# Kernel tuning notes

Hardware: AMD Instinct MI355X
Metric: run time of the kernel (lower is better)

The kernel has to match this reference:

```python
import jax, jax.numpy as jnp
import numpy as np

G = 256          # voxel grid extent per axis
N = 30000        # number of active voxels
CHANNELS = [(4,16),(16,16),(16,32),(32,32),(32,32),(32,64),(64,64),(64,64),(64,64),(64,64),(64,64),(64,64),(64,128)]
BN_EPS = 1e-3

_OFFS = np.array([[i, j, k] for i in (-1, 0, 1) for j in (-1, 0, 1) for k in (-1, 0, 1)], dtype=np.int32)  # 27 kernel taps


def setup_inputs() -> dict:
    key = jax.random.key(0)
    ks = jax.random.split(key, 2 + len(CHANNELS))
    rng = np.random.default_rng(0)
    # unique active voxel coordinates in [0, G)^3
    c = rng.integers(0, G, size=(2 * N, 3))
    c = np.unique(c, axis=0)
    rng.shuffle(c)
    coords = jnp.asarray(c[:N], dtype=jnp.int32)
    inp = {
        "voxel_features": jax.random.normal(ks[0], (N, CHANNELS[0][0]), jnp.float32),
        "coords": coords,
    }
    for i, (ci, co) in enumerate(CHANNELS):
        inp[f"W{i}"] = jax.random.normal(ks[1 + i], (27, ci, co), jnp.float32) * (1.0 / np.sqrt(27.0 * ci))
        inp[f"g{i}"] = jnp.ones((co,), jnp.float32)
        inp[f"b{i}"] = jnp.zeros((co,), jnp.float32)
    return inp


def _neighbors(coords):
    """Build rulebook: for each of 27 taps, index of neighbor voxel (or masked)."""
    n = coords.shape[0]
    grid = jnp.full((G, G, G), -1, jnp.int32).at[coords[:, 0], coords[:, 1], coords[:, 2]].set(
        jnp.arange(n, dtype=jnp.int32))
    offs = jnp.asarray(_OFFS)
    nc = coords[None, :, :] + offs[:, None, :]               # [27, N, 3]
    inb = jnp.all((nc >= 0) & (nc < G), axis=-1)             # [27, N]
    ncc = jnp.clip(nc, 0, G - 1)
    nidx = grid[ncc[..., 0], ncc[..., 1], ncc[..., 2]]       # [27, N]
    valid = (inb & (nidx >= 0)).astype(jnp.float32)
    return jnp.maximum(nidx, 0), valid


def _sconv(feat, W, nidx, valid):
    # gather-GEMM: gathered [27, N, Cin] -> out [N, Cout]
    g = feat[nidx] * valid[..., None]
    return jnp.einsum('knc,kcd->nd', g, W)


def _bn_relu(x, g, b):
    m = jnp.mean(x, axis=0)
    v = jnp.var(x, axis=0)
    return jax.nn.relu((x - m) * jax.lax.rsqrt(v + BN_EPS) * g + b)


def reference(voxel_features, coords,
              W0, W1, W2, W3, W4, W5, W6, W7, W8, W9, W10, W11, W12,
              g0, g1, g2, g3, g4, g5, g6, g7, g8, g9, g10, g11, g12,
              b0, b1, b2, b3, b4, b5, b6, b7, b8, b9, b10, b11, b12):
    Ws = [W0, W1, W2, W3, W4, W5, W6, W7, W8, W9, W10, W11, W12]
    gs = [g0, g1, g2, g3, g4, g5, g6, g7, g8, g9, g10, g11, g12]
    bs = [b0, b1, b2, b3, b4, b5, b6, b7, b8, b9, b10, b11, b12]
    nidx, valid = _neighbors(coords)
    x = voxel_features
    for W, g, b in zip(Ws, gs, bs):
        x = _bn_relu(_sconv(x, W, nidx, valid), g, b)
    return x  # [N, 128] final backbone features
```

## Files before the change

### kernel.cpp

```cpp
#include <hip/hip_runtime.h>
#include <stdint.h>
#include <stddef.h>

#define GG 256

typedef __attribute__((ext_vector_type(8))) short bf16x8;
typedef __attribute__((ext_vector_type(4))) float f32x4;

__device__ __forceinline__ float bf2f(short s) {
  return __builtin_bit_cast(float, ((unsigned)(unsigned short)s) << 16);
}
__device__ __forceinline__ short f2bf(float f) {
  unsigned u = __builtin_bit_cast(unsigned, f);
  unsigned r = (u + 0x7FFFu + ((u >> 16) & 1u)) >> 16;
  return (short)r;
}


__global__ __launch_bounds__(256) void k_clear_grid(uint32_t* g, int n32) {
  int i = blockIdx.x * 256 + threadIdx.x;
  int stride = gridDim.x * 256;
  for (; i < n32; i += stride) g[i] = 0xFFFFFFFFu;
}

__global__ __launch_bounds__(256) void k_scatter(const int* __restrict__ coords,
                                                 uint16_t* __restrict__ grid, int n) {
  int i = blockIdx.x * 256 + threadIdx.x;
  if (i >= n) return;
  int x = coords[3 * i], y = coords[3 * i + 1], z = coords[3 * i + 2];
  grid[(((x << 8) | y) << 8) | z] = (uint16_t)i;
}

__global__ __launch_bounds__(256) void k_rulebook(const int* __restrict__ coords,
                                                  const uint16_t* __restrict__ grid,
                                                  int* __restrict__ nidx, int n) {
  int i = blockIdx.x * 256 + threadIdx.x;
  if (i >= n) return;
  int x = coords[3 * i], y = coords[3 * i + 1], z = coords[3 * i + 2];
  int k = 0;
  for (int dx = -1; dx <= 1; ++dx)
    for (int dy = -1; dy <= 1; ++dy)
      for (int dz = -1; dz <= 1; ++dz) {
        int nx = x + dx, ny = y + dy, nz = z + dz;
        int v = -1;
        if (((nx | ny | nz) >= 0) && nx < GG && ny < GG && nz < GG) {
          uint16_t s = grid[(((nx << 8) | ny) << 8) | nz];
          if (s != 0xFFFFu) v = (int)s;
        }
        nidx[k * n + i] = v;
        ++k;
      }
}


__global__ __launch_bounds__(256) void k_zero(float* __restrict__ stats, float* __restrict__ zp) {
  int i = blockIdx.x * 256 + threadIdx.x;
  if (i < 13 * 256) stats[i] = 0.0f;
  if (i < 64) zp[i] = 0.0f;
}


struct PackArgs {
  const float* W[13];
  short* P[13];
  int ci[13], co[13], nkb[13];
};

__global__ __launch_bounds__(256) void k_pack(PackArgs pa) {
  int L = blockIdx.y;
  int ci = pa.ci[L], co = pa.co[L], nkb = pa.nkb[L];
  int total = nkb * co * 32;
  const float* W = pa.W[L];
  short* P = pa.P[L];
  for (int e = blockIdx.x * 256 + threadIdx.x; e < total; e += gridDim.x * 256) {
    int kk = e & 31;
    int rest = e >> 5;
    int c = rest % co;
    int kb = rest / co;
    int k = kb * 32 + kk;
    int tap = k / ci, cc = k % ci;
    float v = (tap < 27) ? W[((size_t)tap * ci + cc) * co + c] : 0.0f;
    P[e] = f2bf(v);
  }
}


__global__ __launch_bounds__(256) void k_sconv_l0(const float* __restrict__ feat,
                                                  const float* __restrict__ W,
                                                  const int* __restrict__ nidx,
                                                  float* __restrict__ y,
                                                  float* __restrict__ stats, int n) {
  int i = blockIdx.x * 256 + threadIdx.x;
  bool act = i < n;
  int ii = act ? i : (n - 1);
  float acc[16];
#pragma unroll
  for (int c = 0; c < 16; ++c) acc[c] = 0.0f;
  for (int t = 0; t < 27; ++t) {
    int nid = nidx[t * n + ii];
    float4 f = make_float4(0.f, 0.f, 0.f, 0.f);
    if (act && nid >= 0) f = *(const float4*)(feat + 4 * (size_t)nid);
    const float* Wt = W + t * 64;
#pragma unroll
    for (int c = 0; c < 16; ++c)
      acc[c] = fmaf(f.x, Wt[c],
               fmaf(f.y, Wt[16 + c],
               fmaf(f.z, Wt[32 + c],
               fmaf(f.w, Wt[48 + c], acc[c]))));
  }
  if (act) {
    float* o = y + (size_t)i * 16;
#pragma unroll
    for (int c = 0; c < 16; c += 4) *(float4*)(o + c) = make_float4(acc[c], acc[c+1], acc[c+2], acc[c+3]);
  }
  __shared__ float ss[4][16], sq[4][16];
  int w = threadIdx.x >> 6, l = threadIdx.x & 63;
#pragma unroll
  for (int c = 0; c < 16; ++c) {
    float s = act ? acc[c] : 0.0f;
    float q = s * s;
#pragma unroll
    for (int off = 32; off; off >>= 1) {
      s += __shfl_xor(s, off);
      q += __shfl_xor(q, off);
    }
    if (l == 0) { ss[w][c] = s; sq[w][c] = q; }
  }
  __syncthreads();
  if (threadIdx.x < 16) {
    int c = threadIdx.x;
    atomicAdd(&stats[c], ss[0][c] + ss[1][c] + ss[2][c] + ss[3][c]);
    atomicAdd(&stats[16 + c], sq[0][c] + sq[1][c] + sq[2][c] + sq[3][c]);
  }
}


template <int CI, int CO>
__global__ __launch_bounds__(256) void k_sconv_mfma(
    const short* __restrict__ feat, const short* __restrict__ P,
    const int* __restrict__ nidx, const short* __restrict__ zpage,
    short* __restrict__ y, float* __restrict__ stats, int n) {
  constexpr int LOG2CI = (CI == 16) ? 4 : (CI == 32) ? 5 : 6;
  constexpr int NKB = (27 * CI + 31) / 32;
  constexpr int NT = CO / 16;

  const int w = threadIdx.x >> 6;
  const int l = threadIdx.x & 63;
  const int lo = l & 15, g = l >> 4;
  const int bvox = blockIdx.x * 64;
  const int rowg = bvox + 16 * w + lo;
  const int rowc = (rowg < n) ? rowg : (n - 1);

  f32x4 acc[NT];
#pragma unroll
  for (int t = 0; t < NT; ++t) acc[t] = (f32x4){0.f, 0.f, 0.f, 0.f};

  auto loadA = [&](int kb) -> bf16x8 {
    int kg = kb * 32 + 8 * g;
    int tap = kg >> LOG2CI;
    int ch = kg & (CI - 1);
    const short* ap = zpage;
    if (tap < 27) {
      int nid = nidx[tap * n + rowc];
      if (nid >= 0) ap = feat + (size_t)nid * CI + ch;
    }
    return *(const bf16x8*)ap;
  };
  auto loadB = [&](int kb, int t) -> bf16x8 {
    return *(const bf16x8*)(P + ((size_t)(kb * CO + 16 * t + lo)) * 32 + 8 * g);
  };

  bf16x8 a = loadA(0);
  bf16x8 b[NT];
#pragma unroll
  for (int t = 0; t < NT; ++t) b[t] = loadB(0, t);

  for (int kb = 0; kb < NKB - 1; ++kb) {
    bf16x8 an = loadA(kb + 1);
    bf16x8 bn[NT];
#pragma unroll
    for (int t = 0; t < NT; ++t) bn[t] = loadB(kb + 1, t);
#pragma unroll
    for (int t = 0; t < NT; ++t)
      acc[t] = __builtin_amdgcn_mfma_f32_16x16x32_bf16(a, b[t], acc[t], 0, 0, 0);
    a = an;
#pragma unroll
    for (int t = 0; t < NT; ++t) b[t] = bn[t];
  }
#pragma unroll
  for (int t = 0; t < NT; ++t)
    acc[t] = __builtin_amdgcn_mfma_f32_16x16x32_bf16(a, b[t], acc[t], 0, 0, 0);

  __shared__ float ss[4][CO], sq[4][CO];
#pragma unroll
  for (int t = 0; t < NT; ++t) {
    int col = 16 * t + lo;
    float sv = 0.f, qv = 0.f;
#pragma unroll
    for (int r = 0; r < 4; ++r) {
      int row = bvox + 16 * w + 4 * g + r;
      float v = acc[t][r];
      bool valid = row < n;
      if (valid) y[(size_t)row * CO + col] = f2bf(v);
      v = valid ? v : 0.f;
      sv += v;
      qv += v * v;
    }
    sv += __shfl_xor(sv, 16); sv += __shfl_xor(sv, 32);
    qv += __shfl_xor(qv, 16); qv += __shfl_xor(qv, 32);
    if (g == 0) { ss[w][col] = sv; sq[w][col] = qv; }
  }
  __syncthreads();
  for (int c = threadIdx.x; c < CO; c += 256) {
    atomicAdd(&stats[c], ss[0][c] + ss[1][c] + ss[2][c] + ss[3][c]);
    atomicAdd(&stats[CO + c], sq[0][c] + sq[1][c] + sq[2][c] + sq[3][c]);
  }
}


template <int CO, bool INF32, bool OUTF32>
__global__ __launch_bounds__(256) void k_bn_apply(const void* __restrict__ yv,
                                                  const float* __restrict__ stats,
                                                  const float* __restrict__ gam,
                                                  const float* __restrict__ bet,
                                                  void* __restrict__ outv, int n) {
  int idx = blockIdx.x * 256 + threadIdx.x;
  int tot = n * CO / 8;
  if (idx >= tot) return;
  size_t e0 = (size_t)idx * 8;
  int c0 = (int)(e0 & (CO - 1));
  float invn = 1.0f / (float)n;

  float vin[8];
  if (INF32) {
    const float4* p = (const float4*)((const float*)yv + e0);
    float4 u0 = p[0], u1 = p[1];
    vin[0] = u0.x; vin[1] = u0.y; vin[2] = u0.z; vin[3] = u0.w;
    vin[4] = u1.x; vin[5] = u1.y; vin[6] = u1.z; vin[7] = u1.w;
  } else {
    bf16x8 v = *(const bf16x8*)((const short*)yv + e0);
#pragma unroll
    for (int j = 0; j < 8; ++j) vin[j] = bf2f(v[j]);
  }

  float vout[8];
#pragma unroll
  for (int j = 0; j < 8; ++j) {
    int c = c0 + j;
    float m = stats[c] * invn;
    float var = fmaf(-m, m, stats[CO + c] * invn);
    float rstd = rsqrtf(var + 1e-3f);
    float o = fmaf((vin[j] - m) * rstd, gam[c], bet[c]);
    vout[j] = fmaxf(o, 0.0f);
  }

  if (OUTF32) {
    float4* p = (float4*)((float*)outv + e0);
    p[0] = make_float4(vout[0], vout[1], vout[2], vout[3]);
    p[1] = make_float4(vout[4], vout[5], vout[6], vout[7]);
  } else {
    bf16x8 o;
#pragma unroll
    for (int j = 0; j < 8; ++j) o[j] = f2bf(vout[j]);
    *(bf16x8*)((short*)outv + e0) = o;
  }
}


extern "C" void kernel_launch(void* const* d_in, const int* in_sizes, int n_in,
                              void* d_out, int out_size, void* d_ws, size_t ws_size,
                              hipStream_t stream) {
  const float* vf = (const float*)d_in[0];
  const int* coords = (const int*)d_in[1];
  const int n = in_sizes[1] / 3;

  static const int CIs[13] = {4, 16, 16, 32, 32, 32, 64, 64, 64, 64, 64, 64, 64};
  static const int COs[13] = {16, 16, 32, 32, 32, 64, 64, 64, 64, 64, 64, 64, 128};

  char* ws = (char*)d_ws;
  size_t off = 0;
  auto carve = [&](size_t bytes) { void* p = ws + off; off = (off + bytes + 255) & ~(size_t)255; return p; };
  uint16_t* grid = (uint16_t*)carve((size_t)GG * GG * GG * 2);
  int* nidx = (int*)carve((size_t)27 * n * 4);
  short* featA = (short*)carve((size_t)n * 128 * 2);
  short* featB = (short*)carve((size_t)n * 128 * 2);
  short* y = (short*)carve((size_t)n * 128 * 2);
  short* Ppool = (short*)carve((size_t)2 * 1024 * 1024 * 2);
  float* stats = (float*)carve((size_t)13 * 256 * 4);
  float* zpage = (float*)carve(256);

  PackArgs pa;
  {
    size_t poff = 0;
    for (int L = 0; L < 13; ++L) {
      int ci = CIs[L], co = COs[L];
      int nkb = (27 * ci + 31) / 32;
      pa.W[L] = (const float*)d_in[2 + 3 * L];
      pa.P[L] = Ppool + poff;
      pa.ci[L] = ci; pa.co[L] = co; pa.nkb[L] = nkb;
      poff += (size_t)nkb * co * 32;
    }
  }

  const int n32 = GG * GG * GG / 2;
  k_clear_grid<<<2048, 256, 0, stream>>>((uint32_t*)grid, n32);
  k_scatter<<<(n + 255) / 256, 256, 0, stream>>>(coords, grid, n);
  k_rulebook<<<(n + 255) / 256, 256, 0, stream>>>(coords, grid, nidx, n);
  k_zero<<<13, 256, 0, stream>>>(stats, zpage);
  k_pack<<<dim3(128, 13), 256, 0, stream>>>(pa);

  k_sconv_l0<<<(n + 255) / 256, 256, 0, stream>>>(vf, pa.W[0], nidx, (float*)y, stats, n);
  k_bn_apply<16, true, false><<<((n * 16 / 8) + 255) / 256, 256, 0, stream>>>(
      (const void*)y, stats, (const float*)d_in[3], (const float*)d_in[4], (void*)featA, n);

  short* cur = featA;
  short* nxt = featB;
  const int nb64 = (n + 63) / 64;

#define RUN_MFMA(L, CI, CO, LAST)                                                             \
  do {                                                                                        \
    float* st = stats + 256 * (L);                                                            \
    k_sconv_mfma<CI, CO><<<nb64, 256, 0, stream>>>(cur, (const short*)pa.P[L], nidx,          \
                                                   (const short*)zpage, y, st, n);            \
    const float* gg = (const float*)d_in[3 + 3 * (L)];                                        \
    const float* bb = (const float*)d_in[4 + 3 * (L)];                                        \
    int nb = ((n * (CO) / 8) + 255) / 256;                                                    \
    if (LAST) {                                                                               \
      k_bn_apply<CO, false, true><<<nb, 256, 0, stream>>>((const void*)y, st, gg, bb,         \
                                                          (void*)d_out, n);                   \
    } else {                                                                                  \
      k_bn_apply<CO, false, false><<<nb, 256, 0, stream>>>((const void*)y, st, gg, bb,        \
                                                           (void*)nxt, n);                    \
      short* t_ = cur; cur = nxt; nxt = t_;                                                   \
    }                                                                                         \
  } while (0)

  RUN_MFMA(1, 16, 16, false);
  RUN_MFMA(2, 16, 32, false);
  RUN_MFMA(3, 32, 32, false);
  RUN_MFMA(4, 32, 32, false);
  RUN_MFMA(5, 32, 64, false);
  RUN_MFMA(6, 64, 64, false);
  RUN_MFMA(7, 64, 64, false);
  RUN_MFMA(8, 64, 64, false);
  RUN_MFMA(9, 64, 64, false);
  RUN_MFMA(10, 64, 64, false);
  RUN_MFMA(11, 64, 64, false);
  RUN_MFMA(12, 64, 128, true);
#undef RUN_MFMA
}
```

Before: 648.1 us.

## Re-partition sparse conv MFMA kernel across waves and shrink rulebook indices

New measurement: 1.017 ms. +56.9%, slower.

```diff
diff --git a/kernel.cpp b/kernel.cpp
--- a/kernel.cpp
+++ b/kernel.cpp
@@ -3,6 +3,7 @@
 #include <stddef.h>
 
 #define GG 256
+#define STP 16
 
 typedef __attribute__((ext_vector_type(8))) short bf16x8;
 typedef __attribute__((ext_vector_type(4))) float f32x4;
@@ -33,7 +34,7 @@
 
 __global__ __launch_bounds__(256) void k_rulebook(const int* __restrict__ coords,
                                                   const uint16_t* __restrict__ grid,
-                                                  int* __restrict__ nidx, int n) {
+                                                  short* __restrict__ nidx, int n) {
   int i = blockIdx.x * 256 + threadIdx.x;
   if (i >= n) return;
   int x = coords[3 * i], y = coords[3 * i + 1], z = coords[3 * i + 2];
@@ -42,10 +43,10 @@
     for (int dy = -1; dy <= 1; ++dy)
       for (int dz = -1; dz <= 1; ++dz) {
         int nx = x + dx, ny = y + dy, nz = z + dz;
-        int v = -1;
+        short v = -1;
         if (((nx | ny | nz) >= 0) && nx < GG && ny < GG && nz < GG) {
           uint16_t s = grid[(((nx << 8) | ny) << 8) | nz];
-          if (s != 0xFFFFu) v = (int)s;
+          if (s != 0xFFFFu) v = (short)s;
         }
         nidx[k * n + i] = v;
         ++k;
@@ -54,9 +55,9 @@
 
 
 __global__ __launch_bounds__(256) void k_zero(float* __restrict__ stats, float* __restrict__ zp) {
-  int i = blockIdx.x * 256 + threadIdx.x;
-  if (i < 13 * 256) stats[i] = 0.0f;
-  if (i < 64) zp[i] = 0.0f;
+  int tot = 13 * 256 * STP;
+  for (int i = blockIdx.x * 256 + threadIdx.x; i < tot; i += gridDim.x * 256) stats[i] = 0.0f;
+  if (blockIdx.x == 0 && threadIdx.x < 64) zp[threadIdx.x] = 0.0f;
 }
 
 
@@ -87,7 +88,7 @@
 
 __global__ __launch_bounds__(256) void k_sconv_l0(const float* __restrict__ feat,
                                                   const float* __restrict__ W,
-                                                  const int* __restrict__ nidx,
+                                                  const short* __restrict__ nidx,
                                                   float* __restrict__ y,
                                                   float* __restrict__ stats, int n) {
   int i = blockIdx.x * 256 + threadIdx.x;
@@ -129,8 +130,8 @@
   __syncthreads();
   if (threadIdx.x < 16) {
     int c = threadIdx.x;
-    atomicAdd(&stats[c], ss[0][c] + ss[1][c] + ss[2][c] + ss[3][c]);
-    atomicAdd(&stats[16 + c], sq[0][c] + sq[1][c] + sq[2][c] + sq[3][c]);
+    atomicAdd(&stats[c * STP], ss[0][c] + ss[1][c] + ss[2][c] + ss[3][c]);
+    atomicAdd(&stats[(16 + c) * STP], sq[0][c] + sq[1][c] + sq[2][c] + sq[3][c]);
   }
 }
 
@@ -138,22 +139,31 @@
 template <int CI, int CO>
 __global__ __launch_bounds__(256) void k_sconv_mfma(
     const short* __restrict__ feat, const short* __restrict__ P,
-    const int* __restrict__ nidx, const short* __restrict__ zpage,
-    short* __restrict__ y, float* __restrict__ stats, int n) {
+    const short* __restrict__ nidx, const short* __restrict__ zpage,
+    float* __restrict__ y, float* __restrict__ stats, int n) {
   constexpr int LOG2CI = (CI == 16) ? 4 : (CI == 32) ? 5 : 6;
   constexpr int NKB = (27 * CI + 31) / 32;
-  constexpr int NT = CO / 16;
+  constexpr int MT = (CO == 16) ? 4 : (CO == 32) ? 2 : 1;
+  constexpr int WPM = 4 / MT;
+  constexpr int NT = (CO == 128) ? 2 : 1;
+  constexpr int R = MT * 16;
 
   const int w = threadIdx.x >> 6;
   const int l = threadIdx.x & 63;
   const int lo = l & 15, g = l >> 4;
-  const int bvox = blockIdx.x * 64;
-  const int rowg = bvox + 16 * w + lo;
-  const int rowc = (rowg < n) ? rowg : (n - 1);
-
-  f32x4 acc[NT];
-#pragma unroll
-  for (int t = 0; t < NT; ++t) acc[t] = (f32x4){0.f, 0.f, 0.f, 0.f};
+  const int mt = w / WPM;
+  const int nw = w % WPM;
+  const int bvox = blockIdx.x * R;
+
+  __shared__ short nid_s[27][R];
+  for (int idx = threadIdx.x; idx < 27 * R; idx += 256) {
+    int tap = idx / R, r = idx % R;
+    int v = bvox + r;
+    nid_s[tap][r] = (v < n) ? nidx[tap * n + v] : (short)-1;
+  }
+  __syncthreads();
+
+  const int rowl = mt * 16 + lo;
 
   auto loadA = [&](int kb) -> bf16x8 {
     int kg = kb * 32 + 8 * g;
@@ -161,65 +171,76 @@
     int ch = kg & (CI - 1);
     const short* ap = zpage;
     if (tap < 27) {
-      int nid = nidx[tap * n + rowc];
+      int nid = nid_s[tap][rowl];
       if (nid >= 0) ap = feat + (size_t)nid * CI + ch;
     }
     return *(const bf16x8*)ap;
   };
-  auto loadB = [&](int kb, int t) -> bf16x8 {
+  auto loadB = [&](int kb, int j) -> bf16x8 {
+    int t = nw + j * WPM;
     return *(const bf16x8*)(P + ((size_t)(kb * CO + 16 * t + lo)) * 32 + 8 * g);
   };
 
-  bf16x8 a = loadA(0);
-  bf16x8 b[NT];
-#pragma unroll
-  for (int t = 0; t < NT; ++t) b[t] = loadB(0, t);
-
-  for (int kb = 0; kb < NKB - 1; ++kb) {
-    bf16x8 an = loadA(kb + 1);
-    bf16x8 bn[NT];
-#pragma unroll
-    for (int t = 0; t < NT; ++t) bn[t] = loadB(kb + 1, t);
-#pragma unroll
-    for (int t = 0; t < NT; ++t)
-      acc[t] = __builtin_amdgcn_mfma_f32_16x16x32_bf16(a, b[t], acc[t], 0, 0, 0);
-    a = an;
-#pragma unroll
-    for (int t = 0; t < NT; ++t) b[t] = bn[t];
-  }
-#pragma unroll
-  for (int t = 0; t < NT; ++t)
-    acc[t] = __builtin_amdgcn_mfma_f32_16x16x32_bf16(a, b[t], acc[t], 0, 0, 0);
-
-  __shared__ float ss[4][CO], sq[4][CO];
-#pragma unroll
-  for (int t = 0; t < NT; ++t) {
-    int col = 16 * t + lo;
+  f32x4 acc[NT];
+#pragma unroll
+  for (int j = 0; j < NT; ++j) acc[j] = (f32x4){0.f, 0.f, 0.f, 0.f};
+
+  bf16x8 aC = loadA(0), aN = loadA(1);
+  bf16x8 bC[NT], bN[NT];
+#pragma unroll
+  for (int j = 0; j < NT; ++j) { bC[j] = loadB(0, j); bN[j] = loadB(1, j); }
+
+#pragma unroll 2
+  for (int kb = 0; kb < NKB; ++kb) {
+    bf16x8 aP = aC;
+    bf16x8 bP[NT];
+#pragma unroll
+    for (int j = 0; j < NT; ++j) bP[j] = bC[j];
+    if (kb + 2 < NKB) {
+      aP = loadA(kb + 2);
+#pragma unroll
+      for (int j = 0; j < NT; ++j) bP[j] = loadB(kb + 2, j);
+    }
+#pragma unroll
+    for (int j = 0; j < NT; ++j)
+      acc[j] = __builtin_amdgcn_mfma_f32_16x16x32_bf16(aC, bC[j], acc[j], 0, 0, 0);
+    aC = aN; aN = aP;
+#pragma unroll
+    for (int j = 0; j < NT; ++j) { bC[j] = bN[j]; bN[j] = bP[j]; }
+  }
+
+  __shared__ float ss[MT][CO], sq[MT][CO];
+#pragma unroll
+  for (int j = 0; j < NT; ++j) {
+    int col = 16 * (nw + j * WPM) + lo;
     float sv = 0.f, qv = 0.f;
 #pragma unroll
     for (int r = 0; r < 4; ++r) {
-      int row = bvox + 16 * w + 4 * g + r;
-      float v = acc[t][r];
+      int row = bvox + mt * 16 + 4 * g + r;
+      float v = acc[j][r];
       bool valid = row < n;
-      if (valid) y[(size_t)row * CO + col] = f2bf(v);
+      if (valid) y[(size_t)row * CO + col] = v;
       v = valid ? v : 0.f;
       sv += v;
       qv += v * v;
     }
     sv += __shfl_xor(sv, 16); sv += __shfl_xor(sv, 32);
     qv += __shfl_xor(qv, 16); qv += __shfl_xor(qv, 32);
-    if (g == 0) { ss[w][col] = sv; sq[w][col] = qv; }
+    if (g == 0) { ss[mt][col] = sv; sq[mt][col] = qv; }
   }
   __syncthreads();
   for (int c = threadIdx.x; c < CO; c += 256) {
-    atomicAdd(&stats[c], ss[0][c] + ss[1][c] + ss[2][c] + ss[3][c]);
-    atomicAdd(&stats[CO + c], sq[0][c] + sq[1][c] + sq[2][c] + sq[3][c]);
-  }
-}
-
-
-template <int CO, bool INF32, bool OUTF32>
-__global__ __launch_bounds__(256) void k_bn_apply(const void* __restrict__ yv,
+    float s = 0.f, q = 0.f;
+#pragma unroll
+    for (int m = 0; m < MT; ++m) { s += ss[m][c]; q += sq[m][c]; }
+    atomicAdd(&stats[c * STP], s);
+    atomicAdd(&stats[(CO + c) * STP], q);
+  }
+}
+
+
+template <int CO, bool OUTF32>
+__global__ __launch_bounds__(256) void k_bn_apply(const float* __restrict__ yv,
                                                   const float* __restrict__ stats,
                                                   const float* __restrict__ gam,
                                                   const float* __restrict__ bet,
@@ -231,33 +252,25 @@
   int c0 = (int)(e0 & (CO - 1));
   float invn = 1.0f / (float)n;
 
-  float vin[8];
-  if (INF32) {
-    const float4* p = (const float4*)((const float*)yv + e0);
-    float4 u0 = p[0], u1 = p[1];
-    vin[0] = u0.x; vin[1] = u0.y; vin[2] = u0.z; vin[3] = u0.w;
-    vin[4] = u1.x; vin[5] = u1.y; vin[6] = u1.z; vin[7] = u1.w;
-  } else {
-    bf16x8 v = *(const bf16x8*)((const short*)yv + e0);
-#pragma unroll
-    for (int j = 0; j < 8; ++j) vin[j] = bf2f(v[j]);
-  }
+  const float4* p = (const float4*)(yv + e0);
+  float4 u0 = p[0], u1 = p[1];
+  float vin[8] = {u0.x, u0.y, u0.z, u0.w, u1.x, u1.y, u1.z, u1.w};
 
   float vout[8];
 #pragma unroll
   for (int j = 0; j < 8; ++j) {
     int c = c0 + j;
-    float m = stats[c] * invn;
-    float var = fmaf(-m, m, stats[CO + c] * invn);
+    float m = stats[c * STP] * invn;
+    float var = fmaf(-m, m, stats[(CO + c) * STP] * invn);
     float rstd = rsqrtf(var + 1e-3f);
     float o = fmaf((vin[j] - m) * rstd, gam[c], bet[c]);
     vout[j] = fmaxf(o, 0.0f);
   }
 
   if (OUTF32) {
-    float4* p = (float4*)((float*)outv + e0);
-    p[0] = make_float4(vout[0], vout[1], vout[2], vout[3]);
-    p[1] = make_float4(vout[4], vout[5], vout[6], vout[7]);
+    float4* q = (float4*)((float*)outv + e0);
+    q[0] = make_float4(vout[0], vout[1], vout[2], vout[3]);
+    q[1] = make_float4(vout[4], vout[5], vout[6], vout[7]);
   } else {
     bf16x8 o;
 #pragma unroll
@@ -281,12 +294,12 @@
   size_t off = 0;
   auto carve = [&](size_t bytes) { void* p = ws + off; off = (off + bytes + 255) & ~(size_t)255; return p; };
   uint16_t* grid = (uint16_t*)carve((size_t)GG * GG * GG * 2);
-  int* nidx = (int*)carve((size_t)27 * n * 4);
+  short* nidx = (short*)carve((size_t)27 * n * 2);
   short* featA = (short*)carve((size_t)n * 128 * 2);
   short* featB = (short*)carve((size_t)n * 128 * 2);
-  short* y = (short*)carve((size_t)n * 128 * 2);
-  short* Ppool = (short*)carve((size_t)2 * 1024 * 1024 * 2);
-  float* stats = (float*)carve((size_t)13 * 256 * 4);
+  float* y = (float*)carve((size_t)n * 128 * 4);
+  short* Ppool = (short*)carve((size_t)4 * 1024 * 1024);
+  float* stats = (float*)carve((size_t)13 * 256 * STP * 4);
   float* zpage = (float*)carve(256);
 
   PackArgs pa;
@@ -306,31 +319,30 @@
   k_clear_grid<<<2048, 256, 0, stream>>>((uint32_t*)grid, n32);
   k_scatter<<<(n + 255) / 256, 256, 0, stream>>>(coords, grid, n);
   k_rulebook<<<(n + 255) / 256, 256, 0, stream>>>(coords, grid, nidx, n);
-  k_zero<<<13, 256, 0, stream>>>(stats, zpage);
+  k_zero<<<208, 256, 0, stream>>>(stats, zpage);
   k_pack<<<dim3(128, 13), 256, 0, stream>>>(pa);
 
-  k_sconv_l0<<<(n + 255) / 256, 256, 0, stream>>>(vf, pa.W[0], nidx, (float*)y, stats, n);
-  k_bn_apply<16, true, false><<<((n * 16 / 8) + 255) / 256, 256, 0, stream>>>(
-      (const void*)y, stats, (const float*)d_in[3], (const float*)d_in[4], (void*)featA, n);
+  k_sconv_l0<<<(n + 255) / 256, 256, 0, stream>>>(vf, pa.W[0], nidx, y, stats, n);
+  k_bn_apply<16, false><<<((n * 16 / 8) + 255) / 256, 256, 0, stream>>>(
+      y, stats, (const float*)d_in[3], (const float*)d_in[4], (void*)featA, n);
 
   short* cur = featA;
   short* nxt = featB;
-  const int nb64 = (n + 63) / 64;
 
 #define RUN_MFMA(L, CI, CO, LAST)                                                             \
   do {                                                                                        \
-    float* st = stats + 256 * (L);                                                            \
-    k_sconv_mfma<CI, CO><<<nb64, 256, 0, stream>>>(cur, (const short*)pa.P[L], nidx,          \
+    constexpr int MT_ = ((CO) == 16) ? 4 : ((CO) == 32) ? 2 : 1;                              \
+    const int nblk = (n + MT_ * 16 - 1) / (MT_ * 16);                                         \
+    float* st = stats + 256 * STP * (L);                                                      \
+    k_sconv_mfma<CI, CO><<<nblk, 256, 0, stream>>>(cur, (const short*)pa.P[L], nidx,          \
                                                    (const short*)zpage, y, st, n);            \
     const float* gg = (const float*)d_in[3 + 3 * (L)];                                        \
     const float* bb = (const float*)d_in[4 + 3 * (L)];                                        \
     int nb = ((n * (CO) / 8) + 255) / 256;                                                    \
     if (LAST) {                                                                               \
-      k_bn_apply<CO, false, true><<<nb, 256, 0, stream>>>((const void*)y, st, gg, bb,         \
-                                                          (void*)d_out, n);                   \
+      k_bn_apply<CO, true><<<nb, 256, 0, stream>>>(y, st, gg, bb, (void*)d_out, n);           \
     } else {                                                                                  \
-      k_bn_apply<CO, false, false><<<nb, 256, 0, stream>>>((const void*)y, st, gg, bb,        \
-                                                           (void*)nxt, n);                    \
+      k_bn_apply<CO, false><<<nb, 256, 0, stream>>>(y, st, gg, bb, (void*)nxt, n);            \
       short* t_ = cur; cur = nxt; nxt = t_;                                                   \
     }                                                                                         \
   } while (0)
```
